# Kernel optimization log

Hardware: AMD Instinct MI355X
Metric: run time of the kernel (lower is better)

## Reference

```python
import jax, jax.numpy as jnp
import numpy as np

B, N, D_ITEM, D_EMB, N_CLASSES = 32, 8192, 128, 512, 1000

def _linear_params(key, din, dout):
    kw, kb = jax.random.split(key)
    lim = 1.0 / np.sqrt(din)
    w = jax.random.uniform(kw, (dout, din), jnp.float32, -lim, lim)
    b = jax.random.uniform(kb, (dout,), jnp.float32, -lim, lim)
    return w, b

def setup_inputs() -> dict:
    key = jax.random.key(0)
    ks = jax.random.split(key, 11)
    inp = {
        'x_items': jax.random.normal(ks[0], (B, N, D_ITEM), jnp.float32),
        'x_query': jax.random.normal(ks[1], (B, 1), jnp.float32),
    }
    inp['psi_x_w1'], inp['psi_x_b1'] = _linear_params(ks[2], D_ITEM, D_EMB)
    inp['psi_x_w2'], inp['psi_x_b2'] = _linear_params(ks[3], D_EMB, D_EMB)
    inp['psi_q_w1'], inp['psi_q_b1'] = _linear_params(ks[4], 1, D_EMB)
    inp['psi_q_w2'], inp['psi_q_b2'] = _linear_params(ks[5], D_EMB, D_EMB)
    inp['q_w'], inp['q_b'] = _linear_params(ks[6], D_EMB, D_EMB)
    inp['k_w'], inp['k_b'] = _linear_params(ks[7], D_EMB, D_EMB)
    inp['v_w'], inp['v_b'] = _linear_params(ks[8], D_EMB, D_EMB)
    inp['phi_w1'], inp['phi_b1'] = _linear_params(ks[9], D_EMB, D_EMB)
    inp['phi_w2'], inp['phi_b2'] = _linear_params(ks[10], D_EMB, N_CLASSES)
    return inp

def _mlp(x, w1, b1, w2, b2):
    # Linear -> exact GELU (torch nn.GELU default) -> Linear
    h = jax.nn.gelu(x @ w1.T + b1, approximate=False)
    return h @ w2.T + b2

def reference(x_items, x_query,
              psi_x_w1, psi_x_b1, psi_x_w2, psi_x_b2,
              psi_q_w1, psi_q_b1, psi_q_w2, psi_q_b2,
              q_w, q_b, k_w, k_b, v_w, v_b,
              phi_w1, phi_b1, phi_w2, phi_b2):
    h_items = _mlp(x_items, psi_x_w1, psi_x_b1, psi_x_w2, psi_x_b2)      # [B,N,D]
    h_query = _mlp(x_query[..., None], psi_q_w1, psi_q_b1, psi_q_w2, psi_q_b2)  # [B,1,D]
    q = h_query @ q_w.T + q_b                                             # [B,1,D]
    k = h_items @ k_w.T + k_b                                             # [B,N,D]
    v = h_items @ v_w.T + v_b                                             # [B,N,D]
    scores = jnp.einsum('bqd,bnd->bqn', q, k) * (k.shape[-1] ** -0.5)     # [B,1,N]
    attn = jax.nn.softmax(scores, axis=-1)                                # traditional softmax
    z = jnp.einsum('bqn,bnd->bqd', attn, v)[:, 0, :]                      # [B,D]
    return _mlp(z, phi_w1, phi_b1, phi_w2, phi_b2)                        # [B,n_classes]
```

## Files before the change

### kernel.cpp

```cpp
#include <hip/hip_runtime.h>
#include <hip/hip_bf16.h>

#define B_ 32
#define N_ 8192
#define DI_ 128
#define D_ 512
#define NC_ 1000
#define TN_ 128
#define SN_ 32
#define NSUB_ 4
#define NT_ 64
#define XROW_ 136

typedef short s8v __attribute__((ext_vector_type(8)));
typedef float f4v __attribute__((ext_vector_type(4)));

__device__ __forceinline__ unsigned short f2bf(float f){
  union { float f; unsigned u; } c; c.f = f;
  unsigned r = c.u + 0x7fffu + ((c.u >> 16) & 1u);
  return (unsigned short)(r >> 16);
}

__device__ __forceinline__ unsigned pk2bf(float a, float b){
  float2 f; f.x = a; f.y = b;
  __hip_bfloat162 h = __float22bfloat162_rn(f);
  union { __hip_bfloat162 h; unsigned u; } c; c.h = h;
  return c.u;
}

__device__ __forceinline__ float gelu_f(float x){
  float ax = fabsf(x) * 0.70710678118654752f;
  float t = __builtin_amdgcn_rcpf(1.0f + 0.3275911f * ax);
  float poly = ((((1.061405429f*t - 1.453152027f)*t + 1.421413741f)*t
                 - 0.284496736f)*t + 0.254829592f)*t;
  float e = __expf(-ax*ax);
  float erf_ax = 1.0f - poly*e;
  erf_ax = (x >= 0.0f) ? erf_ax : -erf_ax;
  return 0.5f * x * (1.0f + erf_ax);
}

__device__ __forceinline__ float wsum64(float v){
  #pragma unroll
  for (int off = 32; off; off >>= 1) v += __shfl_xor(v, off, 64);
  return v;
}

__global__ __launch_bounds__(512)
void k_prep2(const float* __restrict__ w1, unsigned short* __restrict__ w1p,
             const float* __restrict__ sw0, float* __restrict__ dt0,
             const float* __restrict__ sw1, float* __restrict__ dt1,
             const float* __restrict__ sw2, float* __restrict__ dt2,
             const float* __restrict__ sw3, float* __restrict__ dt3,
             const float* __restrict__ sw4, float* __restrict__ dt4,
             const float* __restrict__ pw2, float* __restrict__ pw2T){
  const int t = threadIdx.x;
  const int bid = blockIdx.x;
  if (bid < 128){
    const int i = bid*512 + t;
    const int j = i / DI_, kc = i % DI_;
    const int kk = kc >> 5, q = (kc >> 3) & 3, s = kc & 7;
    w1p[((kk*D_ + j)*4 + q)*8 + s] = f2bf(w1[i]);
    return;
  }
  __shared__ float tile[64][65];
  const int r0 = t >> 6;
  const int c  = t & 63;
  if (bid < 448){
    const int id = bid - 128;
    const int mi = id >> 6;
    const int tt = id & 63;
    const int to = tt >> 3, tk = tt & 7;
    const float* src = mi==0?sw0: mi==1?sw1: mi==2?sw2: mi==3?sw3: sw4;
    float*       dst = mi==0?dt0: mi==1?dt1: mi==2?dt2: mi==3?dt3: dt4;
    #pragma unroll
    for (int i = 0; i < 8; ++i){
      const int r = r0 + i*8;
      tile[r][c] = src[(size_t)(to*64 + r)*D_ + tk*64 + c];
    }
    __syncthreads();
    #pragma unroll
    for (int i = 0; i < 8; ++i){
      const int r = r0 + i*8;
      dst[(size_t)(tk*64 + r)*D_ + to*64 + c] = tile[c][r];
    }
  } else {
    const int id = bid - 448;
    const int tr = id >> 3, tk = id & 7;
    #pragma unroll
    for (int i = 0; i < 8; ++i){
      const int r = r0 + i*8;
      const int ro = tr*64 + r;
      tile[r][c] = (ro < NC_) ? pw2[(size_t)ro*D_ + tk*64 + c] : 0.f;
    }
    __syncthreads();
    #pragma unroll
    for (int i = 0; i < 8; ++i){
      const int r = r0 + i*8;
      const int co = tr*64 + c;
      if (co < NC_)
        pw2T[(size_t)(tk*64 + r)*NC_ + co] = tile[c][r];
    }
  }
}

template<int J, bool ACT, bool HASB>
__global__ __launch_bounds__(512)
void k_gemv(const float* __restrict__ WT, const float* __restrict__ X,
            const float* __restrict__ bias, float* __restrict__ Y,
            const float scale){
  const int sl = blockIdx.x, b = blockIdx.y, t = threadIdx.x;
  const int c = t & 63, w = t >> 6;
  __shared__ float xs[D_];
  __shared__ float red[8][64];
  xs[t] = X[(size_t)b*D_ + t];
  __syncthreads();
  const int j = sl*64 + c;
  const float* wp = WT + (size_t)(w*64)*J + j;
  const float* xp = xs + w*64;
  float a0=0.f, a1=0.f, a2=0.f, a3=0.f;
  #pragma unroll
  for (int k = 0; k < 64; k += 4){
    a0 += wp[(size_t)(k+0)*J] * xp[k+0];
    a1 += wp[(size_t)(k+1)*J] * xp[k+1];
    a2 += wp[(size_t)(k+2)*J] * xp[k+2];
    a3 += wp[(size_t)(k+3)*J] * xp[k+3];
  }
  red[w][c] = (a0+a1)+(a2+a3);
  __syncthreads();
  if (w == 0 && j < J){
    float s = ((red[0][c]+red[1][c])+(red[2][c]+red[3][c]))
            + ((red[4][c]+red[5][c])+(red[6][c]+red[7][c]));
    s = s * scale;
    if (HASB) s += bias[j];
    Y[(size_t)b*J + j] = ACT ? gelu_f(s) : s;
  }
}

__global__ __launch_bounds__(512)
void k_gemv_q1(const float* __restrict__ xq,  const float* __restrict__ w1q,
               const float* __restrict__ b1q,
               const float* __restrict__ WT,  const float* __restrict__ bias,
               float* __restrict__ Y){
  const int sl = blockIdx.x, b = blockIdx.y, t = threadIdx.x;
  const int c = t & 63, w = t >> 6;
  __shared__ float xs[D_];
  __shared__ float red[8][64];
  xs[t] = gelu_f(xq[b] * w1q[t] + b1q[t]);
  __syncthreads();
  const int j = sl*64 + c;
  const float* wp = WT + (size_t)(w*64)*D_ + j;
  const float* xp = xs + w*64;
  float a0=0.f, a1=0.f, a2=0.f, a3=0.f;
  #pragma unroll
  for (int k = 0; k < 64; k += 4){
    a0 += wp[(size_t)(k+0)*D_] * xp[k+0];
    a1 += wp[(size_t)(k+1)*D_] * xp[k+1];
    a2 += wp[(size_t)(k+2)*D_] * xp[k+2];
    a3 += wp[(size_t)(k+3)*D_] * xp[k+3];
  }
  red[w][c] = (a0+a1)+(a2+a3);
  __syncthreads();
  if (w == 0){
    float s = ((red[0][c]+red[1][c])+(red[2][c]+red[3][c]))
            + ((red[4][c]+red[5][c])+(red[6][c]+red[7][c]));
    Y[(size_t)b*D_ + j] = s + bias[j];
  }
}

__global__ __launch_bounds__(512, 2)
void k_main(const float* __restrict__ x,
            const unsigned short* __restrict__ w1p,
            const float* __restrict__ b1,
            const float* __restrict__ qkw2,
            float* __restrict__ part,
            float* __restrict__ esum){
  const int tile = blockIdx.x;
  const int b = blockIdx.y;
  const int t = threadIdx.x;
  const int lane = t & 63;
  const int wid = t >> 6;
  const int ln = lane & 15;
  const int q  = lane >> 4;

  __shared__ unsigned short x_lds[2][SN_ * XROW_];
  __shared__ float s_ws[8][SN_];
  __shared__ float e_lds[SN_];
  __shared__ float sb1[D_];
  __shared__ float sq2[D_];

  const int jb = wid * 64;
  const unsigned short* w1base = w1p + (jb + ln)*32 + q*8;
  const float* xbase = x + ((size_t)b * N_ + tile * TN_) * DI_;

  sb1[t] = b1[t];
  sq2[t] = qkw2[b*D_ + t];
  {
    const float4* x4 = (const float4*)xbase;
    #pragma unroll
    for (int i = 0; i < 2; ++i){
      const int f = i*512 + t;
      float4 v = x4[f];
      const int m = f >> 5;
      const int k = (f & 31) << 2;
      uint2 pk;
      pk.x = pk2bf(v.x, v.y);
      pk.y = pk2bf(v.z, v.w);
      *(uint2*)&x_lds[0][m*XROW_ + k] = pk;
    }
  }
  __syncthreads();

  f4v zacc[4];
  #pragma unroll
  for (int i = 0; i < 4; ++i) zacc[i] = (f4v){0.f,0.f,0.f,0.f};
  float etot = 0.f;

  for (int s = 0; s < NSUB_; ++s){
    const unsigned short* xb = x_lds[s & 1];

    f4v acc[8];
    #pragma unroll
    for (int i = 0; i < 8; ++i) acc[i] = (f4v){0.f,0.f,0.f,0.f};

    #pragma unroll
    for (int kk = 0; kk < 4; ++kk){
      const int k = kk*32 + q*8;
      s8v aw[4];
      #pragma unroll
      for (int jt = 0; jt < 4; ++jt)
        aw[jt] = *(const s8v*)(w1base + kk*(D_*32) + jt*(16*32));
      s8v bx[2];
      #pragma unroll
      for (int mi = 0; mi < 2; ++mi)
        bx[mi] = *(const s8v*)&xb[(mi*16 + ln)*XROW_ + k];
      #pragma unroll
      for (int jt = 0; jt < 4; ++jt)
        #pragma unroll
        for (int mi = 0; mi < 2; ++mi)
          acc[jt*2+mi] = __builtin_amdgcn_mfma_f32_16x16x32_bf16(aw[jt], bx[mi], acc[jt*2+mi], 0,0,0);
    }

    float4 pv0, pv1;
    if (s + 1 < NSUB_){
      const float4* x4 = (const float4*)(xbase + (size_t)(s+1)*SN_*DI_);
      pv0 = x4[t];
      pv1 = x4[512 + t];
    }

    float sp0 = 0.f, sp1 = 0.f;
    #pragma unroll
    for (int jt = 0; jt < 4; ++jt){
      const f4v bv = *(const f4v*)&sb1[jb + jt*16 + q*4];
      const f4v qv = *(const f4v*)&sq2[jb + jt*16 + q*4];
      #pragma unroll
      for (int mi = 0; mi < 2; ++mi){
        f4v a = acc[jt*2+mi];
        a[0] = gelu_f(a[0] + bv[0]);
        a[1] = gelu_f(a[1] + bv[1]);
        a[2] = gelu_f(a[2] + bv[2]);
        a[3] = gelu_f(a[3] + bv[3]);
        acc[jt*2+mi] = a;
        const float d = qv[0]*a[0] + qv[1]*a[1] + qv[2]*a[2] + qv[3]*a[3];
        if (mi == 0) sp0 += d; else sp1 += d;
      }
    }
    sp0 += __shfl_xor(sp0, 16, 64); sp0 += __shfl_xor(sp0, 32, 64);
    sp1 += __shfl_xor(sp1, 16, 64); sp1 += __shfl_xor(sp1, 32, 64);
    if (q == 0) s_ws[wid][lane] = sp0;
    if (q == 1) s_ws[wid][lane] = sp1;

    if (s + 1 < NSUB_){
      unsigned short* xn = &x_lds[(s+1) & 1][0];
      int f = t, m = f >> 5, k = (f & 31) << 2;
      uint2 pk;
      pk.x = pk2bf(pv0.x, pv0.y);
      pk.y = pk2bf(pv0.z, pv0.w);
      *(uint2*)&xn[m*XROW_ + k] = pk;
      f = 512 + t; m = f >> 5; k = (f & 31) << 2;
      pk.x = pk2bf(pv1.x, pv1.y);
      pk.y = pk2bf(pv1.z, pv1.w);
      *(uint2*)&xn[m*XROW_ + k] = pk;
    }
    __syncthreads();

    if (t < SN_){
      float sc = 0.f;
      #pragma unroll
      for (int w = 0; w < 8; ++w) sc += s_ws[w][t];
      e_lds[t] = __expf(sc);
    }
    __syncthreads();

    if (wid == 0){
      float v = (lane < SN_) ? e_lds[lane] : 0.f;
      etot += wsum64(v);
    }

    {
      const float em0 = e_lds[ln];
      const float em1 = e_lds[16 + ln];
      #pragma unroll
      for (int jt = 0; jt < 4; ++jt){
        const f4v a0 = acc[jt*2+0];
        const f4v a1 = acc[jt*2+1];
        #pragma unroll
        for (int r = 0; r < 4; ++r)
          zacc[jt][r] += em0*a0[r] + em1*a1[r];
      }
    }
  }

  if (t == 0) esum[b*NT_ + tile] = etot;

  #pragma unroll
  for (int jt = 0; jt < 4; ++jt){
    #pragma unroll
    for (int r = 0; r < 4; ++r){
      float v = zacc[jt][r];
      v += __shfl_xor(v, 1, 64);
      v += __shfl_xor(v, 2, 64);
      v += __shfl_xor(v, 4, 64);
      v += __shfl_xor(v, 8, 64);
      zacc[jt][r] = v;
    }
    if (ln == 0){
      float4 o; o.x = zacc[jt][0]; o.y = zacc[jt][1]; o.z = zacc[jt][2]; o.w = zacc[jt][3];
      *(float4*)&part[((size_t)(b*NT_ + tile))*D_ + jb + jt*16 + q*4] = o;
    }
  }
}

__global__ __launch_bounds__(128)
void k_fu(const float* __restrict__ part, const float* __restrict__ esum,
          float* __restrict__ u){
  const int b = blockIdx.x, sl = blockIdx.y, t = threadIdx.x;
  float p = esum[b*NT_ + (t & 63)];
  p = wsum64(p);
  const float linv = 1.0f / p;
  const int col = sl*128 + t;
  const float* pb = part + (size_t)b*NT_*D_ + col;
  float s = 0.f;
  #pragma unroll 8
  for (int tl = 0; tl < NT_; ++tl) s += pb[tl*D_];
  u[b*D_ + col] = s * linv;
}

extern "C" void kernel_launch(void* const* d_in, const int* in_sizes, int n_in,
                              void* d_out, int out_size, void* d_ws, size_t ws_size,
                              hipStream_t stream) {
  (void)in_sizes; (void)n_in; (void)out_size; (void)ws_size;
  const float* x_items  = (const float*)d_in[0];
  const float* x_query  = (const float*)d_in[1];
  const float* psi_x_w1 = (const float*)d_in[2];
  const float* psi_x_b1 = (const float*)d_in[3];
  const float* psi_x_w2 = (const float*)d_in[4];
  const float* psi_x_b2 = (const float*)d_in[5];
  const float* psi_q_w1 = (const float*)d_in[6];
  const float* psi_q_b1 = (const float*)d_in[7];
  const float* psi_q_w2 = (const float*)d_in[8];
  const float* psi_q_b2 = (const float*)d_in[9];
  const float* q_w      = (const float*)d_in[10];
  const float* q_b      = (const float*)d_in[11];
  const float* k_w      = (const float*)d_in[12];
  const float* v_w      = (const float*)d_in[14];
  const float* v_b      = (const float*)d_in[15];
  const float* phi_w1   = (const float*)d_in[16];
  const float* phi_b1   = (const float*)d_in[17];
  const float* phi_w2   = (const float*)d_in[18];
  const float* phi_b2   = (const float*)d_in[19];
  float* out = (float*)d_out;

  char* ws = (char*)d_ws;
  unsigned short* w1p = (unsigned short*)(ws);
  float* qkw2 = (float*)(ws + 131072);
  float* part = (float*)(ws + 196608);
  float* h2g  = (float*)(ws + 196608);
  float* qvg  = (float*)(ws + 262144);
  float* qkg  = (float*)(ws + 327680);
  float* esum = (float*)(ws + 4390912);
  float* w2T  = (float*)(ws + 4399104);
  float* vwT  = (float*)(ws + 5447680);
  float* pw1T = (float*)(ws + 6496256);
  float* w2qT = (float*)(ws + 7544832);
  float* ub   = (float*)(ws + 7544832);
  float* u2b  = (float*)(ws + 7610368);
  float* zb   = (float*)(ws + 7675904);
  float* hb   = (float*)(ws + 7741440);
  float* qwT  = (float*)(ws + 8593408);
  float* pw2T = (float*)(ws + 9641984);

  const float SC = 0.04419417382415922f;

  hipLaunchKernelGGL(k_prep2, dim3(576), dim3(512), 0, stream,
                     psi_x_w1, w1p,
                     psi_x_w2, w2T, v_w, vwT, phi_w1, pw1T,
                     psi_q_w2, w2qT, q_w, qwT, phi_w2, pw2T);
  hipLaunchKernelGGL(k_gemv_q1, dim3(8, 32), dim3(512), 0, stream,
                     x_query, psi_q_w1, psi_q_b1, w2qT, psi_q_b2, h2g);
  hipLaunchKernelGGL(HIP_KERNEL_NAME(k_gemv<D_, false, true>), dim3(8, 32), dim3(512), 0, stream,
                     qwT, h2g, q_b, qvg, 1.0f);
  hipLaunchKernelGGL(HIP_KERNEL_NAME(k_gemv<D_, false, false>), dim3(8, 32), dim3(512), 0, stream,
                     k_w, qvg, q_b , qkg, SC);
  hipLaunchKernelGGL(HIP_KERNEL_NAME(k_gemv<D_, false, false>), dim3(8, 32), dim3(512), 0, stream,
                     psi_x_w2, qkg, q_b , qkw2, 1.0f);
  hipLaunchKernelGGL(k_main, dim3(NT_, B_), dim3(512), 0, stream,
                     x_items, w1p, psi_x_b1, qkw2, part, esum);
  hipLaunchKernelGGL(k_fu, dim3(32, 4), dim3(128), 0, stream,
                     part, esum, ub);
  hipLaunchKernelGGL(HIP_KERNEL_NAME(k_gemv<D_, false, true>), dim3(8, 32), dim3(512), 0, stream,
                     w2T, ub, psi_x_b2, u2b, 1.0f);
  hipLaunchKernelGGL(HIP_KERNEL_NAME(k_gemv<D_, false, true>), dim3(8, 32), dim3(512), 0, stream,
                     vwT, u2b, v_b, zb, 1.0f);
  hipLaunchKernelGGL(HIP_KERNEL_NAME(k_gemv<D_, true, true>), dim3(8, 32), dim3(512), 0, stream,
                     pw1T, zb, phi_b1, hb, 1.0f);
  hipLaunchKernelGGL(HIP_KERNEL_NAME(k_gemv<NC_, false, true>), dim3(16, 32), dim3(512), 0, stream,
                     pw2T, hb, phi_b2, out, 1.0f);
}
```

Baseline: 358.5 us.

## Pre-multiply adjacent weight matrices and shrink main kernel to 256-thread blocks

The prep kernel now computes fused weight products K·W2, (Q·W2q)ᵀ with folded bias, and (V·W2)ᵀ with folded bias using a tiled SGEMM. Chained GEMV launches collapse into single GEMVs: two fewer on the query path and one fewer on the value path. Separately, the main kernel moves to 256 threads with 16-row sub-tiles and 8 column tiles per wave, changing MFMA tiling and register use. The prep now does about three 512³ GEMMs in scalar FP32, which may cost more than the launches it removes. Rounding order also changes.

```diff
diff --git a/kernel.cpp b/kernel.cpp
--- a/kernel.cpp
+++ b/kernel.cpp
@@ -7,8 +7,8 @@
 #define D_ 512
 #define NC_ 1000
 #define TN_ 128
-#define SN_ 32
-#define NSUB_ 4
+#define SN_ 16
+#define NSUB_ 8
 #define NT_ 64
 #define XROW_ 136
 
@@ -46,15 +46,22 @@
 }
 
 __global__ __launch_bounds__(512)
-void k_prep2(const float* __restrict__ w1, unsigned short* __restrict__ w1p,
-             const float* __restrict__ sw0, float* __restrict__ dt0,
-             const float* __restrict__ sw1, float* __restrict__ dt1,
-             const float* __restrict__ sw2, float* __restrict__ dt2,
-             const float* __restrict__ sw3, float* __restrict__ dt3,
-             const float* __restrict__ sw4, float* __restrict__ dt4,
-             const float* __restrict__ pw2, float* __restrict__ pw2T){
+void k_prep3(const float* __restrict__ w1,  unsigned short* __restrict__ w1p,
+             const float* __restrict__ pw1, float* __restrict__ pw1T,
+             const float* __restrict__ pw2, float* __restrict__ pw2T,
+             const float* __restrict__ kw,  const float* __restrict__ w2,
+             float* __restrict__ KW2,
+             const float* __restrict__ qw,  const float* __restrict__ w2q,
+             const float* __restrict__ b2q, const float* __restrict__ qb,
+             float* __restrict__ QW2qT,
+             const float* __restrict__ vw,  const float* __restrict__ b2x,
+             const float* __restrict__ vb,  float* __restrict__ VW2T){
   const int t = threadIdx.x;
   const int bid = blockIdx.x;
+  __shared__ float As[64][65];
+  __shared__ float Bs[64][68];
+  __shared__ float bsv[64];
+
   if (bid < 128){
     const int i = bid*512 + t;
     const int j = i / DI_, kc = i % DI_;
@@ -62,35 +69,32 @@
     w1p[((kk*D_ + j)*4 + q)*8 + s] = f2bf(w1[i]);
     return;
   }
-  __shared__ float tile[64][65];
   const int r0 = t >> 6;
   const int c  = t & 63;
-  if (bid < 448){
+  if (bid < 192){
     const int id = bid - 128;
-    const int mi = id >> 6;
-    const int tt = id & 63;
-    const int to = tt >> 3, tk = tt & 7;
-    const float* src = mi==0?sw0: mi==1?sw1: mi==2?sw2: mi==3?sw3: sw4;
-    float*       dst = mi==0?dt0: mi==1?dt1: mi==2?dt2: mi==3?dt3: dt4;
+    const int to = id >> 3, tk = id & 7;
     #pragma unroll
     for (int i = 0; i < 8; ++i){
       const int r = r0 + i*8;
-      tile[r][c] = src[(size_t)(to*64 + r)*D_ + tk*64 + c];
+      As[r][c] = pw1[(size_t)(to*64 + r)*D_ + tk*64 + c];
     }
     __syncthreads();
     #pragma unroll
     for (int i = 0; i < 8; ++i){
       const int r = r0 + i*8;
-      dst[(size_t)(tk*64 + r)*D_ + to*64 + c] = tile[c][r];
-    }
-  } else {
-    const int id = bid - 448;
+      pw1T[(size_t)(tk*64 + r)*D_ + to*64 + c] = As[c][r];
+    }
+    return;
+  }
+  if (bid < 320){
+    const int id = bid - 192;
     const int tr = id >> 3, tk = id & 7;
     #pragma unroll
     for (int i = 0; i < 8; ++i){
       const int r = r0 + i*8;
       const int ro = tr*64 + r;
-      tile[r][c] = (ro < NC_) ? pw2[(size_t)ro*D_ + tk*64 + c] : 0.f;
+      As[r][c] = (ro < NC_) ? pw2[(size_t)ro*D_ + tk*64 + c] : 0.f;
     }
     __syncthreads();
     #pragma unroll
@@ -98,7 +102,75 @@
       const int r = r0 + i*8;
       const int co = tr*64 + c;
       if (co < NC_)
-        pw2T[(size_t)(tk*64 + r)*NC_ + co] = tile[c][r];
+        pw2T[(size_t)(tk*64 + r)*NC_ + co] = As[c][r];
+    }
+    return;
+  }
+  const int id = bid - 320;
+  const int mi = id >> 6;
+  const int tt = id & 63;
+  const int rt = tt >> 3, ct = tt & 7;
+  const float* A    = (mi==0) ? kw  : (mi==1) ? qw  : vw;
+  const float* B    = (mi==1) ? w2q : w2;
+  const float* bvec = (mi==1) ? b2q : b2x;
+  const float* badd = (mi==1) ? qb  : vb;
+  float* C          = (mi==0) ? KW2 : (mi==1) ? QW2qT : VW2T;
+  const bool nn = (mi == 0);
+  const int arow0 = (nn ? rt : ct) * 64;
+  const int bcol0 = (nn ? ct : rt) * 64;
+
+  float acc[8] = {0.f,0.f,0.f,0.f,0.f,0.f,0.f,0.f};
+  float ba0 = 0.f, ba1 = 0.f;
+
+  for (int i0 = 0; i0 < 512; i0 += 64){
+    #pragma unroll
+    for (int i = 0; i < 8; ++i){
+      const int r = r0 + i*8;
+      As[r][c] = A[(size_t)(arow0 + r)*512 + i0 + c];
+      Bs[r][c] = B[(size_t)(i0 + r)*512 + bcol0 + c];
+    }
+    if (t < 64) bsv[t] = (mi != 0) ? bvec[i0 + t] : 0.f;
+    __syncthreads();
+    if (nn){
+      const int cg = t & 15, rg = t >> 4;
+      #pragma unroll 4
+      for (int ii = 0; ii < 64; ++ii){
+        const float a0 = As[rg*2][ii], a1 = As[rg*2+1][ii];
+        const float4 bv = *(const float4*)&Bs[ii][cg*4];
+        acc[0] += a0*bv.x; acc[1] += a0*bv.y; acc[2] += a0*bv.z; acc[3] += a0*bv.w;
+        acc[4] += a1*bv.x; acc[5] += a1*bv.y; acc[6] += a1*bv.z; acc[7] += a1*bv.w;
+      }
+    } else {
+      const int cg = t & 31, rg = t >> 5;
+      #pragma unroll 4
+      for (int ii = 0; ii < 64; ++ii){
+        const float a0 = As[cg*2][ii], a1 = As[cg*2+1][ii];
+        const float4 bv = *(const float4*)&Bs[ii][rg*4];
+        acc[0] += bv.x*a0; acc[1] += bv.y*a0; acc[2] += bv.z*a0; acc[3] += bv.w*a0;
+        acc[4] += bv.x*a1; acc[5] += bv.y*a1; acc[6] += bv.z*a1; acc[7] += bv.w*a1;
+        if (rg == 0){ const float bb = bsv[ii]; ba0 += a0*bb; ba1 += a1*bb; }
+      }
+    }
+    __syncthreads();
+  }
+  if (nn){
+    const int cg = t & 15, rg = t >> 4;
+    #pragma unroll
+    for (int p = 0; p < 2; ++p){
+      float4 o; o.x = acc[p*4]; o.y = acc[p*4+1]; o.z = acc[p*4+2]; o.w = acc[p*4+3];
+      *(float4*)&C[(size_t)(rt*64 + rg*2 + p)*512 + ct*64 + cg*4] = o;
+    }
+  } else {
+    const int cg = t & 31, rg = t >> 5;
+    #pragma unroll
+    for (int p = 0; p < 4; ++p){
+      float2 o; o.x = acc[p]; o.y = acc[4+p];
+      *(float2*)&C[(size_t)(rt*64 + rg*4 + p)*512 + ct*64 + cg*2] = o;
+    }
+    if (rt == 0 && rg == 0){
+      float* Cb = C + 512*512;
+      Cb[ct*64 + cg*2]     = ba0 + badd[ct*64 + cg*2];
+      Cb[ct*64 + cg*2 + 1] = ba1 + badd[ct*64 + cg*2 + 1];
     }
   }
 }
@@ -167,7 +239,7 @@
   }
 }
 
-__global__ __launch_bounds__(512, 2)
+__global__ __launch_bounds__(256, 2)
 void k_main(const float* __restrict__ x,
             const unsigned short* __restrict__ w1p,
             const float* __restrict__ b1,
@@ -183,22 +255,22 @@
   const int q  = lane >> 4;
 
   __shared__ unsigned short x_lds[2][SN_ * XROW_];
-  __shared__ float s_ws[8][SN_];
+  __shared__ float s_ws[4][SN_];
   __shared__ float e_lds[SN_];
   __shared__ float sb1[D_];
   __shared__ float sq2[D_];
 
-  const int jb = wid * 64;
+  const int jb = wid * 128;
   const unsigned short* w1base = w1p + (jb + ln)*32 + q*8;
   const float* xbase = x + ((size_t)b * N_ + tile * TN_) * DI_;
 
-  sb1[t] = b1[t];
-  sq2[t] = qkw2[b*D_ + t];
+  sb1[t] = b1[t];            sb1[t+256] = b1[t+256];
+  sq2[t] = qkw2[b*D_ + t];   sq2[t+256] = qkw2[b*D_ + t+256];
   {
     const float4* x4 = (const float4*)xbase;
     #pragma unroll
     for (int i = 0; i < 2; ++i){
-      const int f = i*512 + t;
+      const int f = i*256 + t;
       float4 v = x4[f];
       const int m = f >> 5;
       const int k = (f & 31) << 2;
@@ -210,9 +282,9 @@
   }
   __syncthreads();
 
-  f4v zacc[4];
+  f4v zacc[8];
   #pragma unroll
-  for (int i = 0; i < 4; ++i) zacc[i] = (f4v){0.f,0.f,0.f,0.f};
+  for (int i = 0; i < 8; ++i) zacc[i] = (f4v){0.f,0.f,0.f,0.f};
   float etot = 0.f;
 
   for (int s = 0; s < NSUB_; ++s){
@@ -225,49 +297,37 @@
     #pragma unroll
     for (int kk = 0; kk < 4; ++kk){
       const int k = kk*32 + q*8;
-      s8v aw[4];
+      const s8v bx = *(const s8v*)&xb[ln*XROW_ + k];
       #pragma unroll
-      for (int jt = 0; jt < 4; ++jt)
-        aw[jt] = *(const s8v*)(w1base + kk*(D_*32) + jt*(16*32));
-      s8v bx[2];
-      #pragma unroll
-      for (int mi = 0; mi < 2; ++mi)
-        bx[mi] = *(const s8v*)&xb[(mi*16 + ln)*XROW_ + k];
-      #pragma unroll
-      for (int jt = 0; jt < 4; ++jt)
-        #pragma unroll
-        for (int mi = 0; mi < 2; ++mi)
-          acc[jt*2+mi] = __builtin_amdgcn_mfma_f32_16x16x32_bf16(aw[jt], bx[mi], acc[jt*2+mi], 0,0,0);
+      for (int jt = 0; jt < 8; ++jt){
+        const s8v aw = *(const s8v*)(w1base + kk*(D_*32) + jt*(16*32));
+        acc[jt] = __builtin_amdgcn_mfma_f32_16x16x32_bf16(aw, bx, acc[jt], 0,0,0);
+      }
     }
 
     float4 pv0, pv1;
     if (s + 1 < NSUB_){
       const float4* x4 = (const float4*)(xbase + (size_t)(s+1)*SN_*DI_);
       pv0 = x4[t];
-      pv1 = x4[512 + t];
-    }
-
-    float sp0 = 0.f, sp1 = 0.f;
-    #pragma unroll
-    for (int jt = 0; jt < 4; ++jt){
+      pv1 = x4[256 + t];
+    }
+
+    float sp = 0.f;
+    #pragma unroll
+    for (int jt = 0; jt < 8; ++jt){
       const f4v bv = *(const f4v*)&sb1[jb + jt*16 + q*4];
       const f4v qv = *(const f4v*)&sq2[jb + jt*16 + q*4];
-      #pragma unroll
-      for (int mi = 0; mi < 2; ++mi){
-        f4v a = acc[jt*2+mi];
-        a[0] = gelu_f(a[0] + bv[0]);
-        a[1] = gelu_f(a[1] + bv[1]);
-        a[2] = gelu_f(a[2] + bv[2]);
-        a[3] = gelu_f(a[3] + bv[3]);
-        acc[jt*2+mi] = a;
-        const float d = qv[0]*a[0] + qv[1]*a[1] + qv[2]*a[2] + qv[3]*a[3];
-        if (mi == 0) sp0 += d; else sp1 += d;
-      }
-    }
-    sp0 += __shfl_xor(sp0, 16, 64); sp0 += __shfl_xor(sp0, 32, 64);
-    sp1 += __shfl_xor(sp1, 16, 64); sp1 += __shfl_xor(sp1, 32, 64);
-    if (q == 0) s_ws[wid][lane] = sp0;
-    if (q == 1) s_ws[wid][lane] = sp1;
+      f4v a = acc[jt];
+      a[0] = gelu_f(a[0] + bv[0]);
+      a[1] = gelu_f(a[1] + bv[1]);
+      a[2] = gelu_f(a[2] + bv[2]);
+      a[3] = gelu_f(a[3] + bv[3]);
+      acc[jt] = a;
+      sp += qv[0]*a[0] + qv[1]*a[1] + qv[2]*a[2] + qv[3]*a[3];
+    }
+    sp += __shfl_xor(sp, 16, 64);
+    sp += __shfl_xor(sp, 32, 64);
+    if (q == 0) s_ws[wid][ln] = sp;
 
     if (s + 1 < NSUB_){
       unsigned short* xn = &x_lds[(s+1) & 1][0];
@@ -276,7 +336,7 @@
       pk.x = pk2bf(pv0.x, pv0.y);
       pk.y = pk2bf(pv0.z, pv0.w);
       *(uint2*)&xn[m*XROW_ + k] = pk;
-      f = 512 + t; m = f >> 5; k = (f & 31) << 2;
+      f = 256 + t; m = f >> 5; k = (f & 31) << 2;
       pk.x = pk2bf(pv1.x, pv1.y);
       pk.y = pk2bf(pv1.z, pv1.w);
       *(uint2*)&xn[m*XROW_ + k] = pk;
@@ -286,7 +346,7 @@
     if (t < SN_){
       float sc = 0.f;
       #pragma unroll
-      for (int w = 0; w < 8; ++w) sc += s_ws[w][t];
+      for (int w = 0; w < 4; ++w) sc += s_ws[w][t];
       e_lds[t] = __expf(sc);
     }
     __syncthreads();
@@ -297,15 +357,13 @@
     }
 
     {
-      const float em0 = e_lds[ln];
-      const float em1 = e_lds[16 + ln];
+      const float em = e_lds[ln];
       #pragma unroll
-      for (int jt = 0; jt < 4; ++jt){
-        const f4v a0 = acc[jt*2+0];
-        const f4v a1 = acc[jt*2+1];
+      for (int jt = 0; jt < 8; ++jt){
+        const f4v a = acc[jt];
         #pragma unroll
         for (int r = 0; r < 4; ++r)
-          zacc[jt][r] += em0*a0[r] + em1*a1[r];
+          zacc[jt][r] += em * a[r];
       }
     }
   }
@@ -313,7 +371,7 @@
   if (t == 0) esum[b*NT_ + tile] = etot;
 
   #pragma unroll
-  for (int jt = 0; jt < 4; ++jt){
+  for (int jt = 0; jt < 8; ++jt){
     #pragma unroll
     for (int r = 0; r < 4; ++r){
       float v = zacc[jt][r];
@@ -372,45 +430,36 @@
 
   char* ws = (char*)d_ws;
   unsigned short* w1p = (unsigned short*)(ws);
-  float* qkw2 = (float*)(ws + 131072);
-  float* part = (float*)(ws + 196608);
-  float* h2g  = (float*)(ws + 196608);
-  float* qvg  = (float*)(ws + 262144);
-  float* qkg  = (float*)(ws + 327680);
-  float* esum = (float*)(ws + 4390912);
-  float* w2T  = (float*)(ws + 4399104);
-  float* vwT  = (float*)(ws + 5447680);
-  float* pw1T = (float*)(ws + 6496256);
-  float* w2qT = (float*)(ws + 7544832);
-  float* ub   = (float*)(ws + 7544832);
-  float* u2b  = (float*)(ws + 7610368);
-  float* zb   = (float*)(ws + 7675904);
-  float* hb   = (float*)(ws + 7741440);
-  float* qwT  = (float*)(ws + 8593408);
-  float* pw2T = (float*)(ws + 9641984);
+  float* qkw2  = (float*)(ws + 131072);
+  float* part  = (float*)(ws + 196608);
+  float* qvg   = (float*)(ws + 196608);
+  float* esum  = (float*)(ws + 4390912);
+  float* KW2   = (float*)(ws + 4399104);
+  float* ub    = (float*)(ws + 4399104);
+  float* zb    = (float*)(ws + 4464640);
+  float* hb    = (float*)(ws + 4530176);
+  float* QW2qT = (float*)(ws + 5447680);
+  float* VW2T  = (float*)(ws + 6498304);
+  float* pw1T  = (float*)(ws + 7548928);
+  float* pw2T  = (float*)(ws + 8597504);
 
   const float SC = 0.04419417382415922f;
 
-  hipLaunchKernelGGL(k_prep2, dim3(576), dim3(512), 0, stream,
-                     psi_x_w1, w1p,
-                     psi_x_w2, w2T, v_w, vwT, phi_w1, pw1T,
-                     psi_q_w2, w2qT, q_w, qwT, phi_w2, pw2T);
+  hipLaunchKernelGGL(k_prep3, dim3(512), dim3(512), 0, stream,
+                     psi_x_w1, w1p, phi_w1, pw1T, phi_w2, pw2T,
+                     k_w, psi_x_w2, KW2,
+                     q_w, psi_q_w2, psi_q_b2, q_b, QW2qT,
+                     v_w, psi_x_b2, v_b, VW2T);
   hipLaunchKernelGGL(k_gemv_q1, dim3(8, 32), dim3(512), 0, stream,
-                     x_query, psi_q_w1, psi_q_b1, w2qT, psi_q_b2, h2g);
-  hipLaunchKernelGGL(HIP_KERNEL_NAME(k_gemv<D_, false, true>), dim3(8, 32), dim3(512), 0, stream,
-                     qwT, h2g, q_b, qvg, 1.0f);
+                     x_query, psi_q_w1, psi_q_b1, QW2qT, QW2qT + 512*512, qvg);
   hipLaunchKernelGGL(HIP_KERNEL_NAME(k_gemv<D_, false, false>), dim3(8, 32), dim3(512), 0, stream,
-                     k_w, qvg, q_b , qkg, SC);
-  hipLaunchKernelGGL(HIP_KERNEL_NAME(k_gemv<D_, false, false>), dim3(8, 32), dim3(512), 0, stream,
-                     psi_x_w2, qkg, q_b , qkw2, 1.0f);
-  hipLaunchKernelGGL(k_main, dim3(NT_, B_), dim3(512), 0, stream,
+                     KW2, qvg, q_b , qkw2, SC);
+  hipLaunchKernelGGL(k_main, dim3(NT_, B_), dim3(256), 0, stream,
                      x_items, w1p, psi_x_b1, qkw2, part, esum);
   hipLaunchKernelGGL(k_fu, dim3(32, 4), dim3(128), 0, stream,
                      part, esum, ub);
   hipLaunchKernelGGL(HIP_KERNEL_NAME(k_gemv<D_, false, true>), dim3(8, 32), dim3(512), 0, stream,
-                     w2T, ub, psi_x_b2, u2b, 1.0f);
-  hipLaunchKernelGGL(HIP_KERNEL_NAME(k_gemv<D_, false, true>), dim3(8, 32), dim3(512), 0, stream,
-                     vwT, u2b, v_b, zb, 1.0f);
+                     VW2T, ub, VW2T + 512*512, zb, 1.0f);
   hipLaunchKernelGGL(HIP_KERNEL_NAME(k_gemv<D_, true, true>), dim3(8, 32), dim3(512), 0, stream,
                      pw1T, zb, phi_b1, hb, 1.0f);
   hipLaunchKernelGGL(HIP_KERNEL_NAME(k_gemv<NC_, false, true>), dim3(16, 32), dim3(512), 0, stream,
```

After: 383.8 us. 1.07x slower.

## Halve item subtile to 16 rows and raise occupancy to four blocks per CU

Applied to the files above, without the earlier changes.

Shrinks each sub-iteration from 32 to 16 item rows, doubling the number of sub-steps per tile. It halves the MFMA accumulator count and removes the second x-row fragment, and raises the launch-bounds hint from 2 to 4 blocks per CU to cut register pressure and improve latency hiding. The cost is twice as many barriers and score reductions per tile, and each W1 fragment loaded from global memory is now reused across only one x fragment instead of two, so W1 traffic doubles.

```diff
diff --git a/kernel.cpp b/kernel.cpp
--- a/kernel.cpp
+++ b/kernel.cpp
@@ -7,8 +7,8 @@
 #define D_ 512
 #define NC_ 1000
 #define TN_ 128
-#define SN_ 32
-#define NSUB_ 4
+#define SN_ 16
+#define NSUB_ 8
 #define NT_ 64
 #define XROW_ 136
 
@@ -167,7 +167,7 @@
   }
 }
 
-__global__ __launch_bounds__(512, 2)
+__global__ __launch_bounds__(512, 4)
 void k_main(const float* __restrict__ x,
             const unsigned short* __restrict__ w1p,
             const float* __restrict__ b1,
@@ -196,17 +196,13 @@
   sq2[t] = qkw2[b*D_ + t];
   {
     const float4* x4 = (const float4*)xbase;
-    #pragma unroll
-    for (int i = 0; i < 2; ++i){
-      const int f = i*512 + t;
-      float4 v = x4[f];
-      const int m = f >> 5;
-      const int k = (f & 31) << 2;
-      uint2 pk;
-      pk.x = pk2bf(v.x, v.y);
-      pk.y = pk2bf(v.z, v.w);
-      *(uint2*)&x_lds[0][m*XROW_ + k] = pk;
-    }
+    float4 v = x4[t];
+    const int m = t >> 5;
+    const int k = (t & 31) << 2;
+    uint2 pk;
+    pk.x = pk2bf(v.x, v.y);
+    pk.y = pk2bf(v.z, v.w);
+    *(uint2*)&x_lds[0][m*XROW_ + k] = pk;
   }
   __syncthreads();
 
@@ -218,67 +214,49 @@
   for (int s = 0; s < NSUB_; ++s){
     const unsigned short* xb = x_lds[s & 1];
 
-    f4v acc[8];
-    #pragma unroll
-    for (int i = 0; i < 8; ++i) acc[i] = (f4v){0.f,0.f,0.f,0.f};
+    f4v acc[4];
+    #pragma unroll
+    for (int i = 0; i < 4; ++i) acc[i] = (f4v){0.f,0.f,0.f,0.f};
 
     #pragma unroll
     for (int kk = 0; kk < 4; ++kk){
       const int k = kk*32 + q*8;
-      s8v aw[4];
+      const s8v bx = *(const s8v*)&xb[ln*XROW_ + k];
       #pragma unroll
-      for (int jt = 0; jt < 4; ++jt)
-        aw[jt] = *(const s8v*)(w1base + kk*(D_*32) + jt*(16*32));
-      s8v bx[2];
-      #pragma unroll
-      for (int mi = 0; mi < 2; ++mi)
-        bx[mi] = *(const s8v*)&xb[(mi*16 + ln)*XROW_ + k];
-      #pragma unroll
-      for (int jt = 0; jt < 4; ++jt)
-        #pragma unroll
-        for (int mi = 0; mi < 2; ++mi)
-          acc[jt*2+mi] = __builtin_amdgcn_mfma_f32_16x16x32_bf16(aw[jt], bx[mi], acc[jt*2+mi], 0,0,0);
-    }
-
-    float4 pv0, pv1;
-    if (s + 1 < NSUB_){
-      const float4* x4 = (const float4*)(xbase + (size_t)(s+1)*SN_*DI_);
-      pv0 = x4[t];
-      pv1 = x4[512 + t];
-    }
-
-    float sp0 = 0.f, sp1 = 0.f;
+      for (int jt = 0; jt < 4; ++jt){
+        const s8v aw = *(const s8v*)(w1base + kk*(D_*32) + jt*(16*32));
+        acc[jt] = __builtin_amdgcn_mfma_f32_16x16x32_bf16(aw, bx, acc[jt], 0,0,0);
+      }
+    }
+
+    float4 pv0 = make_float4(0.f, 0.f, 0.f, 0.f);
+    if (s + 1 < NSUB_)
+      pv0 = ((const float4*)(xbase + (size_t)(s+1)*SN_*DI_))[t];
+
+    float sp = 0.f;
     #pragma unroll
     for (int jt = 0; jt < 4; ++jt){
       const f4v bv = *(const f4v*)&sb1[jb + jt*16 + q*4];
       const f4v qv = *(const f4v*)&sq2[jb + jt*16 + q*4];
-      #pragma unroll
-      for (int mi = 0; mi < 2; ++mi){
-        f4v a = acc[jt*2+mi];
-        a[0] = gelu_f(a[0] + bv[0]);
-        a[1] = gelu_f(a[1] + bv[1]);
-        a[2] = gelu_f(a[2] + bv[2]);
-        a[3] = gelu_f(a[3] + bv[3]);
-        acc[jt*2+mi] = a;
-        const float d = qv[0]*a[0] + qv[1]*a[1] + qv[2]*a[2] + qv[3]*a[3];
-        if (mi == 0) sp0 += d; else sp1 += d;
-      }
-    }
-    sp0 += __shfl_xor(sp0, 16, 64); sp0 += __shfl_xor(sp0, 32, 64);
-    sp1 += __shfl_xor(sp1, 16, 64); sp1 += __shfl_xor(sp1, 32, 64);
-    if (q == 0) s_ws[wid][lane] = sp0;
-    if (q == 1) s_ws[wid][lane] = sp1;
+      f4v a = acc[jt];
+      a[0] = gelu_f(a[0] + bv[0]);
+      a[1] = gelu_f(a[1] + bv[1]);
+      a[2] = gelu_f(a[2] + bv[2]);
+      a[3] = gelu_f(a[3] + bv[3]);
+      acc[jt] = a;
+      sp += qv[0]*a[0] + qv[1]*a[1] + qv[2]*a[2] + qv[3]*a[3];
+    }
+    sp += __shfl_xor(sp, 16, 64);
+    sp += __shfl_xor(sp, 32, 64);
+    if (q == 0) s_ws[wid][ln] = sp;
 
     if (s + 1 < NSUB_){
       unsigned short* xn = &x_lds[(s+1) & 1][0];
-      int f = t, m = f >> 5, k = (f & 31) << 2;
+      const int m = t >> 5;
+      const int k = (t & 31) << 2;
       uint2 pk;
       pk.x = pk2bf(pv0.x, pv0.y);
       pk.y = pk2bf(pv0.z, pv0.w);
-      *(uint2*)&xn[m*XROW_ + k] = pk;
-      f = 512 + t; m = f >> 5; k = (f & 31) << 2;
-      pk.x = pk2bf(pv1.x, pv1.y);
-      pk.y = pk2bf(pv1.z, pv1.w);
       *(uint2*)&xn[m*XROW_ + k] = pk;
     }
     __syncthreads();
@@ -297,15 +275,13 @@
     }
 
     {
-      const float em0 = e_lds[ln];
-      const float em1 = e_lds[16 + ln];
+      const float em = e_lds[ln];
       #pragma unroll
       for (int jt = 0; jt < 4; ++jt){
-        const f4v a0 = acc[jt*2+0];
-        const f4v a1 = acc[jt*2+1];
+        const f4v a = acc[jt];
         #pragma unroll
         for (int r = 0; r < 4; ++r)
-          zacc[jt][r] += em0*a0[r] + em1*a1[r];
+          zacc[jt][r] += em * a[r];
       }
     }
   }
```

After: 398.8 us. +11.3%, slower.
